# Kernel tuning notes

Hardware: AMD Instinct MI355X
Metric: run time of the kernel (lower is better)

Reference implementation:

```python
import jax, jax.numpy as jnp
import numpy as np

KH, KW = 3, 3  # kernel_size from init_kwargs
PH, PW = (KH - 1) // 2, (KW - 1) // 2  # zero padding, same as _compute_zero_padding


def _window_features(x):
    # Equivalent to F.conv2d with the one-hot (binary) kernel, groups=C:
    # extracts each of the KH*KW shifted views with zero padding.
    # x: [B, C, H, W] -> [B, C, KH*KW, H, W]
    b, c, h, w = x.shape
    xp = jnp.pad(x, ((0, 0), (0, 0), (PH, PH), (PW, PW)))
    views = [xp[:, :, i:i + h, j:j + w] for i in range(KH) for j in range(KW)]
    return jnp.stack(views, axis=2)


def setup_inputs() -> dict:
    key = jax.random.key(0)
    x = jax.random.normal(key, (8, 16, 512, 512), dtype=jnp.float32)
    return {"x": x}


def reference(x):
    # features: [B, C, KH*KW, H, W]; reduce_method='median'
    feats = _window_features(x)
    # KH*KW = 9 is odd, so jnp.median (middle of sorted) matches torch.median
    return jnp.median(feats, axis=2)
```

## Files before the change

### kernel.cpp

```cpp
#include <hip/hip_runtime.h>


#define WD 512
#define HT 512
#define PLANE (WD * HT)

__device__ __forceinline__ void s2(float& a, float& b) {
    float t = fminf(a, b);
    b = fmaxf(a, b);
    a = t;
}

__device__ __forceinline__ float med9(float p0, float p1, float p2,
                                      float p3, float p4, float p5,
                                      float p6, float p7, float p8) {
    s2(p1, p2); s2(p4, p5); s2(p7, p8);
    s2(p0, p1); s2(p3, p4); s2(p6, p7);
    s2(p1, p2); s2(p4, p5); s2(p7, p8);
    s2(p0, p3); s2(p5, p8); s2(p4, p7);
    s2(p3, p6); s2(p1, p4); s2(p2, p5);
    s2(p4, p7); s2(p4, p2); s2(p6, p4);
    s2(p4, p2);
    return p4;
}

__global__ __launch_bounds__(256)
void medblur3x3(const float* __restrict__ in, float* __restrict__ out) {
    int t = blockIdx.x * blockDim.x + threadIdx.x;
    int plane = t >> 16;
    int idx   = (t & 0xFFFF) << 2;
    int h  = idx >> 9;
    int w0 = idx & 511;

    const float* base = in + (long)plane * PLANE;

    float r[3][6];
#pragma unroll
    for (int dr = 0; dr < 3; ++dr) {
        int hh = h + dr - 1;
        if (hh < 0 || hh >= HT) {
#pragma unroll
            for (int j = 0; j < 6; ++j) r[dr][j] = 0.0f;
        } else {
            const float* row = base + hh * WD;
            float4 c = *reinterpret_cast<const float4*>(row + w0);
            r[dr][1] = c.x; r[dr][2] = c.y; r[dr][3] = c.z; r[dr][4] = c.w;
            r[dr][0] = (w0 == 0)        ? 0.0f : row[w0 - 1];
            r[dr][5] = (w0 == WD - 4)   ? 0.0f : row[w0 + 4];
        }
    }

    float4 o;
    o.x = med9(r[0][0], r[0][1], r[0][2],
               r[1][0], r[1][1], r[1][2],
               r[2][0], r[2][1], r[2][2]);
    o.y = med9(r[0][1], r[0][2], r[0][3],
               r[1][1], r[1][2], r[1][3],
               r[2][1], r[2][2], r[2][3]);
    o.z = med9(r[0][2], r[0][3], r[0][4],
               r[1][2], r[1][3], r[1][4],
               r[2][2], r[2][3], r[2][4]);
    o.w = med9(r[0][3], r[0][4], r[0][5],
               r[1][3], r[1][4], r[1][5],
               r[2][3], r[2][4], r[2][5]);

    *reinterpret_cast<float4*>(out + (long)plane * PLANE + idx) = o;
}

extern "C" void kernel_launch(void* const* d_in, const int* in_sizes, int n_in,
                              void* d_out, int out_size, void* d_ws, size_t ws_size,
                              hipStream_t stream) {
    const float* x = (const float*)d_in[0];
    float* out = (float*)d_out;

    int nthreads = out_size / 4;
    int block = 256;
    int grid = nthreads / block;
    medblur3x3<<<grid, block, 0, stream>>>(x, out);
}
```

Measured before the change: 236.4 us.

## Use column-sort median-of-9 with fmed3 and wave shuffles for halo

```diff
diff --git a/kernel.cpp b/kernel.cpp
--- a/kernel.cpp
+++ b/kernel.cpp
@@ -5,66 +5,64 @@
 #define HT 512
 #define PLANE (WD * HT)
 
-__device__ __forceinline__ void s2(float& a, float& b) {
-    float t = fminf(a, b);
-    b = fmaxf(a, b);
-    a = t;
-}
-
-__device__ __forceinline__ float med9(float p0, float p1, float p2,
-                                      float p3, float p4, float p5,
-                                      float p6, float p7, float p8) {
-    s2(p1, p2); s2(p4, p5); s2(p7, p8);
-    s2(p0, p1); s2(p3, p4); s2(p6, p7);
-    s2(p1, p2); s2(p4, p5); s2(p7, p8);
-    s2(p0, p3); s2(p5, p8); s2(p4, p7);
-    s2(p3, p6); s2(p1, p4); s2(p2, p5);
-    s2(p4, p7); s2(p4, p2); s2(p6, p4);
-    s2(p4, p2);
-    return p4;
-}
+__device__ __forceinline__ float min3f(float a, float b, float c) { return fminf(fminf(a, b), c); }
+__device__ __forceinline__ float max3f(float a, float b, float c) { return fmaxf(fmaxf(a, b), c); }
+__device__ __forceinline__ float med3f(float a, float b, float c) { return __builtin_amdgcn_fmed3f(a, b, c); }
 
 __global__ __launch_bounds__(256)
 void medblur3x3(const float* __restrict__ in, float* __restrict__ out) {
-    int t = blockIdx.x * blockDim.x + threadIdx.x;
-    int plane = t >> 16;
-    int idx   = (t & 0xFFFF) << 2;
-    int h  = idx >> 9;
-    int w0 = idx & 511;
+    int g = blockIdx.x * blockDim.x + threadIdx.x;
+    int lane  = g & 63;
+    int wave  = g >> 6;
+    int row   = wave & (HT - 1);
+    int plane = wave >> 9;
+    int w0 = lane << 3;
 
     const float* base = in + (long)plane * PLANE;
 
-    float r[3][6];
+    float v[3][8];
 #pragma unroll
     for (int dr = 0; dr < 3; ++dr) {
-        int hh = h + dr - 1;
-        if (hh < 0 || hh >= HT) {
+        int hh = row + dr - 1;
+        if (hh >= 0 && hh < HT) {
+            const float4* rp = reinterpret_cast<const float4*>(base + hh * WD + w0);
+            float4 a = rp[0], b = rp[1];
+            v[dr][0] = a.x; v[dr][1] = a.y; v[dr][2] = a.z; v[dr][3] = a.w;
+            v[dr][4] = b.x; v[dr][5] = b.y; v[dr][6] = b.z; v[dr][7] = b.w;
+        } else {
 #pragma unroll
-            for (int j = 0; j < 6; ++j) r[dr][j] = 0.0f;
-        } else {
-            const float* row = base + hh * WD;
-            float4 c = *reinterpret_cast<const float4*>(row + w0);
-            r[dr][1] = c.x; r[dr][2] = c.y; r[dr][3] = c.z; r[dr][4] = c.w;
-            r[dr][0] = (w0 == 0)        ? 0.0f : row[w0 - 1];
-            r[dr][5] = (w0 == WD - 4)   ? 0.0f : row[w0 + 4];
+            for (int j = 0; j < 8; ++j) v[dr][j] = 0.0f;
         }
     }
 
-    float4 o;
-    o.x = med9(r[0][0], r[0][1], r[0][2],
-               r[1][0], r[1][1], r[1][2],
-               r[2][0], r[2][1], r[2][2]);
-    o.y = med9(r[0][1], r[0][2], r[0][3],
-               r[1][1], r[1][2], r[1][3],
-               r[2][1], r[2][2], r[2][3]);
-    o.z = med9(r[0][2], r[0][3], r[0][4],
-               r[1][2], r[1][3], r[1][4],
-               r[2][2], r[2][3], r[2][4]);
-    o.w = med9(r[0][3], r[0][4], r[0][5],
-               r[1][3], r[1][4], r[1][5],
-               r[2][3], r[2][4], r[2][5]);
+    float lo[10], mi[10], hi[10];
+#pragma unroll
+    for (int j = 0; j < 8; ++j) {
+        lo[j + 1] = min3f(v[0][j], v[1][j], v[2][j]);
+        mi[j + 1] = med3f(v[0][j], v[1][j], v[2][j]);
+        hi[j + 1] = max3f(v[0][j], v[1][j], v[2][j]);
+    }
+    lo[0] = __shfl_up(lo[8], 1, 64);
+    mi[0] = __shfl_up(mi[8], 1, 64);
+    hi[0] = __shfl_up(hi[8], 1, 64);
+    lo[9] = __shfl_down(lo[1], 1, 64);
+    mi[9] = __shfl_down(mi[1], 1, 64);
+    hi[9] = __shfl_down(hi[1], 1, 64);
+    if (lane == 0)  { lo[0] = 0.0f; mi[0] = 0.0f; hi[0] = 0.0f; }
+    if (lane == 63) { lo[9] = 0.0f; mi[9] = 0.0f; hi[9] = 0.0f; }
 
-    *reinterpret_cast<float4*>(out + (long)plane * PLANE + idx) = o;
+    float o[8];
+#pragma unroll
+    for (int j = 0; j < 8; ++j) {
+        float a = max3f(lo[j], lo[j + 1], lo[j + 2]);
+        float b = med3f(mi[j], mi[j + 1], mi[j + 2]);
+        float c = min3f(hi[j], hi[j + 1], hi[j + 2]);
+        o[j] = med3f(a, b, c);
+    }
+
+    float* op = out + (long)plane * PLANE + row * WD + w0;
+    reinterpret_cast<float4*>(op)[0] = make_float4(o[0], o[1], o[2], o[3]);
+    reinterpret_cast<float4*>(op)[1] = make_float4(o[4], o[5], o[6], o[7]);
 }
 
 extern "C" void kernel_launch(void* const* d_in, const int* in_sizes, int n_in,
@@ -73,7 +71,7 @@
     const float* x = (const float*)d_in[0];
     float* out = (float*)d_out;
 
-    int nthreads = out_size / 4;
+    int nthreads = out_size / 8;
     int block = 256;
     int grid = nthreads / block;
     medblur3x3<<<grid, block, 0, stream>>>(x, out);
```

Measured after the change: 225.7 us. -4.5%, faster.
